# Optimization experiments

Measured on AMD Instinct MI355X. Metric: run time of the kernel, lower is better.

## Reference

```python
import jax, jax.numpy as jnp
import numpy as np

NUM_SAMPLES = 9


def _resize1d(x, out_size, axis):
    """Bilinear (align_corners=False) resize along one axis, matching torch."""
    in_size = x.shape[axis]
    scale = in_size / out_size
    dst = jnp.arange(out_size, dtype=jnp.float32)
    src = jnp.maximum((dst + 0.5) * scale - 0.5, 0.0)
    i0 = jnp.floor(src).astype(jnp.int32)
    w1 = (src - i0).astype(x.dtype)
    i0 = jnp.clip(i0, 0, in_size - 1)
    i1 = jnp.clip(i0 + 1, 0, in_size - 1)
    x0 = jnp.take(x, i0, axis=axis)
    x1 = jnp.take(x, i1, axis=axis)
    wshape = [1] * x.ndim
    wshape[axis] = out_size
    w1 = w1.reshape(wshape)
    return x0 * (1.0 - w1) + x1 * w1


def _rel_to_abs(x, ns):
    # x: (b, h, l, ns+l-1) -> (b, h, l, ns) via the pad/reshape skew trick
    b, h, l, c = x.shape
    x = jnp.pad(x, ((0, 0), (0, 0), (0, 0), (0, 1)))
    x = x.reshape(b, h, l * (c + 1))
    x = jnp.pad(x, ((0, 0), (0, 0), (0, ns - 1)))
    x = x.reshape(b, h, l + 1, ns + l - 1)
    return x[:, :, :l, l - 1:]


def _relative_logits_1d(q, rel_k, ns):
    # q: (b, heads, x, y, d); rel_k: (y+ns-1, d)
    logits = jnp.einsum('bhxyd,rd->bhxyr', q, rel_k)
    b, h, x, y, r = logits.shape
    logits = logits.reshape(b, h * x, y, r)
    return _rel_to_abs(logits, ns)


def setup_inputs() -> dict:
    key = jax.random.key(0)
    k1, k2, k3 = jax.random.split(key, 3)
    B, heads, Hh, Ww, d = 16, 8, 64, 64, 64
    scale = d ** (-0.5)
    q = jax.random.normal(k1, (B, heads, Hh, Ww, d), dtype=jnp.float32)
    rel_height = jax.random.normal(k2, (Hh + NUM_SAMPLES - 1, d), dtype=jnp.float32) * scale
    rel_width = jax.random.normal(k3, (Ww + NUM_SAMPLES - 1, d), dtype=jnp.float32) * scale
    return {"q": q, "H": Hh, "W": Ww, "rel_height": rel_height, "rel_width": rel_width}


def reference(q, H, W, rel_height, rel_width):
    ns = NUM_SAMPLES
    heads = q.shape[1]
    # bilinear resize of learned tables along the positional axis
    # (the dim_head axis is resized to its own size -> identity)
    rel_w = _resize1d(rel_width, W + ns - 1, axis=0)
    rel_h = _resize1d(rel_height, H + ns - 1, axis=0)

    rel_logits_w = _relative_logits_1d(q, rel_w, ns)          # (b, heads*H, W, ns)
    qT = jnp.swapaxes(q, 2, 3)                                # (b, heads, W, H, d)
    rel_logits_h = _relative_logits_1d(qT, rel_h, ns)         # (b, heads*W, H, ns)

    # torch interpolates (b, ns, heads*W, H) -> (heads*H, W); separable bilinear
    rel_logits_h = _resize1d(rel_logits_h, heads * H, axis=1)
    rel_logits_h = _resize1d(rel_logits_h, W, axis=2)
    return rel_logits_w + rel_logits_h
```

## Files before the change

kernel.cpp:

```cpp
#include <hip/hip_runtime.h>
#include <stdint.h>

#define NS 9

typedef _Float16 f16x8 __attribute__((ext_vector_type(8)));
typedef float    f32x4 __attribute__((ext_vector_type(4)));

#define SBAR __builtin_amdgcn_sched_barrier(0)
#define WAIT_VM(N) do { SBAR; asm volatile("s_waitcnt vmcnt(" #N ")" ::: "memory"); SBAR; } while (0)
#define WAIT_LGKM(N) do { SBAR; asm volatile("s_waitcnt lgkmcnt(" #N ")" ::: "memory"); SBAR; } while (0)

__device__ __forceinline__ unsigned int pk(float a, float b) {
    return __builtin_bit_cast(unsigned int, __builtin_amdgcn_cvt_pkrtz(a, b));
}


__global__ __launch_bounds__(512, 2) void relpos_kernel(
    const float* __restrict__ q,
    const float* __restrict__ relh,
    const float* __restrict__ relw,
    float* __restrict__ out)
{
    __shared__ uint4 S1[16][16][8];
    __shared__ uint4 S2[16][16][8];
    __shared__ uint4 RL[2][2][32][8];

    const int blk = blockIdx.x;
    const int bh  = blk & 127;
    const int wid = blk >> 7;
    const int ta  = wid < 4 ? 0 : wid < 7 ? 1 : wid < 9 ? 2 : 3;
    const int tc  = wid < 4 ? wid : wid < 7 ? wid - 3 : wid < 9 ? wid - 5 : 3;
    const int Ta0 = ta << 4, Tc0 = tc << 4;

    const int t    = threadIdx.x;
    const int lane = t & 63;
    const int wvu  = __builtin_amdgcn_readfirstlane(t >> 6);
    const int wg   = wvu >> 2;
    const int wl   = wvu & 3;
    const int jl   = lane & 15;
    const int k4p  = lane >> 4;

    const float* __restrict__ qs = q + ((size_t)bh << 18);

    float4 sA[8], sB[8], sR[3];
#pragma unroll
    for (int i = 0; i < 8; ++i) {
        const int F = (i << 9) + t;
        const int al = F >> 8, cc = (F >> 4) & 15, g = F & 15;
        sA[i] = *(const float4*)(qs + (size_t)(Ta0 + al) * 4096
                                    + (size_t)(Tc0 + cc) * 64 + (g << 2));
    }
    SBAR;
#pragma unroll
    for (int i = 0; i < 8; ++i) {
        const int F = (i << 9) + t;
        const int al = F >> 8, cc = (F >> 4) & 15, g = F & 15;
        sB[i] = *(const float4*)(qs + (size_t)(Tc0 + al) * 4096
                                    + (size_t)(Ta0 + cc) * 64 + (g << 2));
    }
    SBAR;
#pragma unroll
    for (int m = 0; m < 3; ++m) {
        const int F = (m << 9) + t;
        const int win = F >= 768;
        const int r = F - (win ? 768 : 0);
        const int tbl = r >= 384;
        const int rr = r - (tbl ? 384 : 0);
        const int row = rr >> 4, g = rr & 15;
        const int rb0 = win ? (48 - Ta0) : (48 - Tc0);
        int gr = rb0 + row; if (gr > 71) gr = 71;
        sR[m] = *(const float4*)((tbl ? relw : relh) + (size_t)gr * 64 + (g << 2));
    }
    SBAR;

    WAIT_VM(11);
#pragma unroll
    for (int i = 0; i < 8; ++i) {
        const int F = (i << 9) + t;
        const int al = F >> 8, cc = (F >> 4) & 15, g = F & 15;
        const int slot = (g >> 1) ^ ((al ^ cc) & 7), half = g & 1;
        uint2 w; w.x = pk(sA[i].x, sA[i].y); w.y = pk(sA[i].z, sA[i].w);
        ((uint2*)&S1[al][cc][slot])[half] = w;
    }
    WAIT_VM(3);
#pragma unroll
    for (int i = 0; i < 8; ++i) {
        const int F = (i << 9) + t;
        const int al = F >> 8, cc = (F >> 4) & 15, g = F & 15;
        const int slot = (g >> 1) ^ ((al ^ cc) & 7), half = g & 1;
        uint2 w; w.x = pk(sB[i].x, sB[i].y); w.y = pk(sB[i].z, sB[i].w);
        ((uint2*)&S2[al][cc][slot])[half] = w;
    }
    WAIT_VM(0);
#pragma unroll
    for (int m = 0; m < 3; ++m) {
        const int F = (m << 9) + t;
        const int win = F >= 768;
        const int r = F - (win ? 768 : 0);
        const int tbl = r >= 384;
        const int rr = r - (tbl ? 384 : 0);
        const int row = rr >> 4, g = rr & 15;
        const int slot = (g >> 1) ^ (row & 7), half = g & 1;
        uint2 w; w.x = pk(sR[m].x, sR[m].y); w.y = pk(sR[m].z, sR[m].w);
        ((uint2*)&RL[win][tbl][row][slot])[half] = w;
    }
    WAIT_LGKM(0);
    __builtin_amdgcn_s_barrier();

    const bool active = (wg == 0) || (ta != tc);
    f32x4 acc[4];
#pragma unroll
    for (int it = 0; it < 4; ++it) acc[it] = (f32x4){0.f, 0.f, 0.f, 0.f};

    if (active) {
        const uint4 (*P)[16][8] = wg ? S2 : S1;
        const uint4 (*Q)[16][8] = wg ? S1 : S2;
        const int win = wg;

        uint4 A0[4], B0[4], A1[4], B1[4];
        auto RD = [&](int r, uint4* A, uint4* B) {
            const int kh = (r & 1) << 2;
#pragma unroll
            for (int it = 0; it < 4; ++it) {
                const int cl = (wl << 2) | it;
                const int sx = (jl ^ cl) & 7;
                A[it] = (r < 2) ? P[jl][cl][(kh + k4p) ^ sx]
                                : Q[cl][jl][(kh + k4p) ^ sx];
                const int rl = (15 - cl) + jl;
                B[it] = RL[win][r < 2 ? 1 : 0][rl][(kh + k4p) ^ (rl & 7)];
            }
        };
        auto MF = [&](const uint4* A, const uint4* B) {
#pragma unroll
            for (int it = 0; it < 4; ++it)
                acc[it] = __builtin_amdgcn_mfma_f32_16x16x32_f16(
                    __builtin_bit_cast(f16x8, A[it]),
                    __builtin_bit_cast(f16x8, B[it]), acc[it], 0, 0, 0);
        };
        RD(0, A0, B0); RD(1, A1, B1);
        WAIT_LGKM(8);  MF(A0, B0);  RD(2, A0, B0);
        WAIT_LGKM(8);  MF(A1, B1);  RD(3, A1, B1);
        WAIT_LGKM(8);  MF(A0, B0);
        WAIT_LGKM(0);  MF(A1, B1);
    }

    __builtin_amdgcn_s_barrier();
    float* OT = (float*)&S1[0][0][0];
    if (active && jl < NS) {
        const int ar = k4p << 2;
#pragma unroll
        for (int it = 0; it < 4; ++it) {
            const int cbase = (((wl << 2) | it) * NS) + jl;
#pragma unroll
            for (int r = 0; r < 4; ++r)
                OT[wg * 2368 + (ar + r) * 148 + cbase] = acc[it][r];
        }
    }
    WAIT_LGKM(0);
    __builtin_amdgcn_s_barrier();

    const int nt = (ta != tc) ? 1152 : 576;
    const size_t ob = (size_t)bh << 6;
    for (int F = t; F < nt; F += 512) {
        const int tile = F >= 576;
        const int rem  = F - (tile ? 576 : 0);
        const int row  = rem / 36;
        const int seg  = rem - row * 36;
        const int Arow0 = tile ? Tc0 : Ta0;
        const int Ccol0 = tile ? Ta0 : Tc0;
        const float4 v = *(const float4*)(OT + tile * 2368 + row * 148 + (seg << 2));
        *(float4*)(out + ((ob + (Arow0 + row)) * 64 + Ccol0) * NS + (seg << 2)) = v;
    }
}

extern "C" void kernel_launch(void* const* d_in, const int* in_sizes, int n_in,
                              void* d_out, int out_size, void* d_ws, size_t ws_size,
                              hipStream_t stream) {
    const float* q    = (const float*)d_in[0];
    const float* relh = (const float*)d_in[3];
    const float* relw = (const float*)d_in[4];
    float* out = (float*)d_out;

    relpos_kernel<<<dim3(1280), dim3(512), 0, stream>>>(q, relh, relw, out);
}
```

Baseline: 32.98 us.

## Pack diagonal tile pairs into one block and store results directly to global

Before this change, each diagonal 16x16 tile pair got its own block, and half of its waves sat idle. Now two diagonal tiles are packed into one block, which cuts the grid from 1280 to 1024 blocks so every wave group does useful MFMA work. The epilogue no longer stages results through LDS with two barriers. Each lane writes its scalar outputs straight to global memory, which saves LDS traffic and syncs but gives less coalesced, strided 4-byte stores.

```diff
diff --git a/kernel.cpp b/kernel.cpp
--- a/kernel.cpp
+++ b/kernel.cpp
@@ -28,9 +28,16 @@
     const int blk = blockIdx.x;
     const int bh  = blk & 127;
     const int wid = blk >> 7;
-    const int ta  = wid < 4 ? 0 : wid < 7 ? 1 : wid < 9 ? 2 : 3;
-    const int tc  = wid < 4 ? wid : wid < 7 ? wid - 3 : wid < 9 ? wid - 5 : 3;
-    const int Ta0 = ta << 4, Tc0 = tc << 4;
+    const bool dpack = (wid >= 6);
+    int RA, CA, RB, CB;
+    if (!dpack) {
+        const int ta = wid < 3 ? 0 : wid < 5 ? 1 : 2;
+        const int tc = wid < 3 ? wid + 1 : wid < 5 ? wid - 1 : 3;
+        RA = ta << 4; CA = tc << 4; RB = CA; CB = RA;
+    } else {
+        const int t0 = (wid - 6) << 1;
+        RA = CA = t0 << 4; RB = CB = (t0 + 1) << 4;
+    }
 
     const int t    = threadIdx.x;
     const int lane = t & 63;
@@ -47,16 +54,16 @@
     for (int i = 0; i < 8; ++i) {
         const int F = (i << 9) + t;
         const int al = F >> 8, cc = (F >> 4) & 15, g = F & 15;
-        sA[i] = *(const float4*)(qs + (size_t)(Ta0 + al) * 4096
-                                    + (size_t)(Tc0 + cc) * 64 + (g << 2));
+        sA[i] = *(const float4*)(qs + (size_t)(RA + al) * 4096
+                                    + (size_t)(CA + cc) * 64 + (g << 2));
     }
     SBAR;
 #pragma unroll
     for (int i = 0; i < 8; ++i) {
         const int F = (i << 9) + t;
         const int al = F >> 8, cc = (F >> 4) & 15, g = F & 15;
-        sB[i] = *(const float4*)(qs + (size_t)(Tc0 + al) * 4096
-                                    + (size_t)(Ta0 + cc) * 64 + (g << 2));
+        sB[i] = *(const float4*)(qs + (size_t)(RB + al) * 4096
+                                    + (size_t)(CB + cc) * 64 + (g << 2));
     }
     SBAR;
 #pragma unroll
@@ -67,7 +74,7 @@
         const int tbl = r >= 384;
         const int rr = r - (tbl ? 384 : 0);
         const int row = rr >> 4, g = rr & 15;
-        const int rb0 = win ? (48 - Ta0) : (48 - Tc0);
+        const int rb0 = win ? (48 - CB) : (48 - CA);
         int gr = rb0 + row; if (gr > 71) gr = 71;
         sR[m] = *(const float4*)((tbl ? relw : relh) + (size_t)gr * 64 + (g << 2));
     }
@@ -107,15 +114,12 @@
     WAIT_LGKM(0);
     __builtin_amdgcn_s_barrier();
 
-    const bool active = (wg == 0) || (ta != tc);
-    f32x4 acc[4];
-#pragma unroll
-    for (int it = 0; it < 4; ++it) acc[it] = (f32x4){0.f, 0.f, 0.f, 0.f};
-
-    if (active) {
+    {
         const uint4 (*P)[16][8] = wg ? S2 : S1;
-        const uint4 (*Q)[16][8] = wg ? S1 : S2;
-        const int win = wg;
+        const uint4 (*Q)[16][8] = dpack ? P : (wg ? S1 : S2);
+        const int win   = wg;
+        const int Arow0 = wg ? RB : RA;
+        const int Ccol0 = wg ? CB : CA;
 
         uint4 A0[4], B0[4], A1[4], B1[4];
         auto RD = [&](int r, uint4* A, uint4* B) {
@@ -130,6 +134,9 @@
                 B[it] = RL[win][r < 2 ? 1 : 0][rl][(kh + k4p) ^ (rl & 7)];
             }
         };
+        f32x4 acc[4];
+#pragma unroll
+        for (int it = 0; it < 4; ++it) acc[it] = (f32x4){0.f, 0.f, 0.f, 0.f};
         auto MF = [&](const uint4* A, const uint4* B) {
 #pragma unroll
             for (int it = 0; it < 4; ++it)
@@ -142,34 +149,18 @@
         WAIT_LGKM(8);  MF(A1, B1);  RD(3, A1, B1);
         WAIT_LGKM(8);  MF(A0, B0);
         WAIT_LGKM(0);  MF(A1, B1);
-    }
 
-    __builtin_amdgcn_s_barrier();
-    float* OT = (float*)&S1[0][0][0];
-    if (active && jl < NS) {
-        const int ar = k4p << 2;
+        if (jl < NS) {
+            const int ar = k4p << 2;
+            const size_t ob = (size_t)bh << 6;
 #pragma unroll
-        for (int it = 0; it < 4; ++it) {
-            const int cbase = (((wl << 2) | it) * NS) + jl;
+            for (int it = 0; it < 4; ++it) {
+                const int cl = (wl << 2) | it;
 #pragma unroll
-            for (int r = 0; r < 4; ++r)
-                OT[wg * 2368 + (ar + r) * 148 + cbase] = acc[it][r];
+                for (int r = 0; r < 4; ++r)
+                    out[((ob + (Arow0 + ar + r)) * 64 + (Ccol0 + cl)) * NS + jl] = acc[it][r];
+            }
         }
-    }
-    WAIT_LGKM(0);
-    __builtin_amdgcn_s_barrier();
-
-    const int nt = (ta != tc) ? 1152 : 576;
-    const size_t ob = (size_t)bh << 6;
-    for (int F = t; F < nt; F += 512) {
-        const int tile = F >= 576;
-        const int rem  = F - (tile ? 576 : 0);
-        const int row  = rem / 36;
-        const int seg  = rem - row * 36;
-        const int Arow0 = tile ? Tc0 : Ta0;
-        const int Ccol0 = tile ? Ta0 : Tc0;
-        const float4 v = *(const float4*)(OT + tile * 2368 + row * 148 + (seg << 2));
-        *(float4*)(out + ((ob + (Arow0 + row)) * 64 + Ccol0) * NS + (seg << 2)) = v;
     }
 }
 
@@ -181,5 +172,5 @@
     const float* relw = (const float*)d_in[4];
     float* out = (float*)d_out;
 
-    relpos_kernel<<<dim3(1280), dim3(512), 0, stream>>>(q, relh, relw, out);
+    relpos_kernel<<<dim3(1024), dim3(512), 0, stream>>>(q, relh, relw, out);
 }
```

Result: faster. 29.82 us (-9.6%).
